# Kernel tuning notes

Measured on AMD Instinct MI355X. Metric: run time of the kernel, lower is better.

The kernel has to match this reference:

```python
import jax, jax.numpy as jnp
import numpy as np

P = 2048       # output dim (genes)
D = 64         # latent dim
H1, H2 = 512, 512  # n_neurons
E = 16         # num_experts
N = 2048       # batch
GATE_H = 64    # gate hidden width


def _glorot(key, shape):
    fan_in, fan_out = shape[-2], shape[-1]
    lim = jnp.sqrt(6.0 / (fan_in + fan_out)).astype(jnp.float32)
    return jax.random.uniform(key, shape, jnp.float32, -lim, lim)


def setup_inputs() -> dict:
    key = jax.random.key(0)
    ks = jax.random.split(key, 12)
    z = jax.random.normal(ks[0], (N, D), jnp.float32)
    # stacked per-expert MLP weights: d -> H1 -> H2 -> p
    W1 = _glorot(ks[1], (E, D, H1));  b1 = jnp.zeros((E, H1), jnp.float32)
    W2 = _glorot(ks[2], (E, H1, H2)); b2 = jnp.zeros((E, H2), jnp.float32)
    W3 = _glorot(ks[3], (E, H2, P));  b3 = jnp.zeros((E, P), jnp.float32)
    # gate network: d -> 64 -> E
    Wg1 = _glorot(ks[4], (D, GATE_H)); bg1 = jnp.zeros((GATE_H,), jnp.float32)
    Wg2 = _glorot(ks[5], (GATE_H, E)); bg2 = jnp.zeros((E,), jnp.float32)
    # expert assignment matrix A: [p, E], binary; ensure no all-zero row
    u = jax.random.uniform(ks[6], (P, E))
    A = jnp.where(u < 0.5, 1.0, 0.0).astype(jnp.float32)
    A = A.at[:, 0].set(1.0)
    return {"z": z, "W1": W1, "b1": b1, "W2": W2, "b2": b2,
            "W3": W3, "b3": b3, "Wg1": Wg1, "bg1": bg1,
            "Wg2": Wg2, "bg2": bg2, "A": A}


def reference(z, W1, b1, W2, b2, W3, b3, Wg1, bg1, Wg2, bg2, A):
    # experts, batched across E (replaces Python loop over nn.ModuleList)
    h = jax.nn.relu(jnp.einsum('nd,edh->neh', z, W1) + b1[None])      # [N,E,H1]
    h = jax.nn.relu(jnp.einsum('neh,ehk->nek', h, W2) + b2[None])     # [N,E,H2]
    expert_out = jnp.einsum('nek,ekp->nep', h, W3) + b3[None]         # [N,E,P]
    # gate network + softmax over experts
    g = jax.nn.relu(z @ Wg1 + bg1) @ Wg2 + bg2                        # [N,E]
    gate = jax.nn.softmax(g, axis=1)                                  # [N,E]
    # feature-wise gating: gate[n,e] * A[p,e], normalized over experts
    fw = gate[:, None, :] * A[None, :, :]                             # [N,P,E]
    fw = fw / (jnp.sum(fw, axis=2, keepdims=True) + 1e-8)
    # weighted combine: sum_e expert_out[n,e,p] * fw[n,p,e]
    x_rec = jnp.einsum('nep,npe->np', expert_out, fw)                 # [N,P]
    return (x_rec, fw)
```

## Files before the change

kernel.cpp:

```cpp
#include <hip/hip_runtime.h>
#include <hip/hip_bf16.h>

#define NN   2048
#define DD   64
#define HH1  512
#define HH2  512
#define PP   2048
#define EE   16

typedef unsigned short ushort_t;
typedef __attribute__((ext_vector_type(8))) short bf16x8;
typedef __attribute__((ext_vector_type(4))) float f32x4;

__device__ __forceinline__ float b2f(ushort_t u) {
  union { unsigned int i; float f; } v; v.i = ((unsigned int)u) << 16; return v.f;
}
__device__ __forceinline__ ushort_t f2b(float f) {
  union { float f; unsigned int i; } v; v.f = f;
  unsigned int x = v.i;
  unsigned int r = (x + 0x7fffu + ((x >> 16) & 1u)) >> 16;
  return (ushort_t)r;
}
__device__ __forceinline__ float ldf(const void* p, size_t i, int isb) {
  return isb ? b2f(((const ushort_t*)p)[i]) : ((const float*)p)[i];
}

__device__ __forceinline__ void async16(ushort_t* lds, const ushort_t* g) {
  __builtin_amdgcn_global_load_lds(
      (const __attribute__((address_space(1))) void*)g,
      (__attribute__((address_space(3))) void*)lds, 16, 0, 0);
}

__global__ void k_sniff(const unsigned int* __restrict__ zraw,
                        int* __restrict__ flag) {
  __shared__ int cnt[256];
  int t = threadIdx.x;
  int c = 0;
  for (int i = t; i < 1024; i += 256) {
    unsigned int u = zraw[i];
    unsigned int e = (u >> 7) & 0xFFu;
    c += (e >= 110u && e <= 135u) ? 1 : 0;
  }
  cnt[t] = c;
  __syncthreads();
  for (int s = 128; s > 0; s >>= 1) {
    if (t < s) cnt[t] += cnt[t + s];
    __syncthreads();
  }
  if (t == 0) *flag = (cnt[0] >= 512) ? 1 : 0;
}

__global__ void k_probe(int* __restrict__ mapflag) {
  __shared__ ushort_t Ap[16 * 32];
  __shared__ ushort_t Bp[16 * 32];
  int t = threadIdx.x;
  for (int i = t; i < 512; i += 64) {
    int r = i >> 5, k = i & 31;
    Ap[i] = f2b((float)((r + k) % 7));
    Bp[i] = f2b((float)((2 * r + k) % 5));
  }
  __syncthreads();
  int lr = t & 15, quad = t >> 4;
  bf16x8 a = *(const bf16x8*)&Ap[lr * 32 + quad * 8];
  bf16x8 b = *(const bf16x8*)&Bp[lr * 32 + quad * 8];
  f32x4 acc = {};
  acc = __builtin_amdgcn_mfma_f32_16x16x32_bf16(a, b, acc, 0, 0, 0);
  bool m0 = true, m1 = true;
  for (int r = 0; r < 4; ++r) {
    float r0 = 0.f, r1 = 0.f;
    for (int k = 0; k < 32; ++k) {
      r0 += (float)(((quad * 4 + r) + k) % 7) * (float)((2 * lr + k) % 5);
      r1 += (float)((lr + k) % 7) * (float)((2 * (quad * 4 + r) + k) % 5);
    }
    m0 &= fabsf(acc[r] - r0) < 0.5f;
    m1 &= fabsf(acc[r] - r1) < 0.5f;
  }
  unsigned long long b0 = __ballot(m0);
  unsigned long long b1 = __ballot(m1);
  if (t == 0) *mapflag = (b0 == ~0ULL) ? 0 : ((b1 == ~0ULL) ? 1 : 0);
}

__global__ void k_convert(const void* __restrict__ src,
                          ushort_t* __restrict__ dst, int n,
                          const int* __restrict__ flag) {
  int isb = *flag;
  int stride = gridDim.x * blockDim.x;
  for (int g = blockIdx.x * blockDim.x + threadIdx.x; g * 8 < n; g += stride) {
    int base = g * 8;
    ushort_t ov[8];
    if (isb) {
      *(uint4*)ov = *(const uint4*)((const ushort_t*)src + base);
    } else {
      const float* s = (const float*)src + base;
      float4 f0 = *(const float4*)s;
      float4 f1 = *(const float4*)(s + 4);
      ov[0] = f2b(f0.x); ov[1] = f2b(f0.y); ov[2] = f2b(f0.z); ov[3] = f2b(f0.w);
      ov[4] = f2b(f1.x); ov[5] = f2b(f1.y); ov[6] = f2b(f1.z); ov[7] = f2b(f1.w);
    }
    *(uint4*)(dst + base) = *(uint4*)ov;
  }
}

__global__ void k_transpose_cvt(const void* __restrict__ src_,
                                ushort_t* __restrict__ dst, int K, int H,
                                const int* __restrict__ flag) {
  __shared__ ushort_t tile[64][68];
  int isb = *flag;
  int e = blockIdx.z;
  size_t ebase = (size_t)e * K * H;
  dst += ebase;
  int h0 = blockIdx.x * 64, k0 = blockIdx.y * 64;
  int t = threadIdx.x;
#pragma unroll
  for (int it = 0; it < 2; ++it) {
    int c = it * 256 + t;
    int row = c >> 3, col = (c & 7) * 8;
    size_t idx = ebase + (size_t)(k0 + row) * H + h0 + col;
    ushort_t tmp[8];
    if (isb) {
      *(uint4*)tmp = *(const uint4*)((const ushort_t*)src_ + idx);
    } else {
      const float* s = (const float*)src_ + idx;
      float4 f0 = *(const float4*)s;
      float4 f1 = *(const float4*)(s + 4);
      tmp[0] = f2b(f0.x); tmp[1] = f2b(f0.y); tmp[2] = f2b(f0.z); tmp[3] = f2b(f0.w);
      tmp[4] = f2b(f1.x); tmp[5] = f2b(f1.y); tmp[6] = f2b(f1.z); tmp[7] = f2b(f1.w);
    }
#pragma unroll
    for (int j = 0; j < 8; ++j) tile[row][col + j] = tmp[j];
  }
  __syncthreads();
#pragma unroll
  for (int it = 0; it < 2; ++it) {
    int c = it * 256 + t;
    int row = c >> 3, col = (c & 7) * 8;
    ushort_t tmp[8];
#pragma unroll
    for (int j = 0; j < 8; ++j) tmp[j] = tile[col + j][row];
    *(uint4*)(dst + (size_t)(h0 + row) * K + k0 + col) = *(uint4*)tmp;
  }
}

__global__ void k_gate(const void* __restrict__ z,
                       const void* __restrict__ Wg1,
                       const void* __restrict__ bg1,
                       const void* __restrict__ Wg2,
                       const void* __restrict__ bg2,
                       const int* __restrict__ flag,
                       float* __restrict__ gate) {
  __shared__ float sW1[64][65];
  __shared__ float sW2[64][16];
  __shared__ float sb1[64];
  __shared__ float sb2[16];
  __shared__ float sz[4][64];
  __shared__ float shid[4][64];
  __shared__ float sg[4][16];
  int isb = *flag;
  int t = threadIdx.x;
  for (int i = t; i < 64 * 64; i += 256) sW1[i >> 6][i & 63] = ldf(Wg1, i, isb);
  for (int i = t; i < 64 * 16; i += 256) sW2[i >> 4][i & 15] = ldf(Wg2, i, isb);
  if (t < 64) sb1[t] = ldf(bg1, t, isb);
  if (t < 16) sb2[t] = ldf(bg2, t, isb);
  int w = t >> 6, l = t & 63;
  int n = blockIdx.x * 4 + w;
  sz[w][l] = ldf(z, (size_t)n * DD + l, isb);
  __syncthreads();
  float acc = sb1[l];
#pragma unroll
  for (int d = 0; d < 64; ++d) acc += sz[w][d] * sW1[d][l];
  shid[w][l] = fmaxf(acc, 0.f);
  __syncthreads();
  if (l < 16) {
    float g = sb2[l];
#pragma unroll
    for (int j = 0; j < 64; ++j) g += shid[w][j] * sW2[j][l];
    sg[w][l] = g;
  }
  __syncthreads();
  if (l < 16) {
    float m = -1e30f;
    for (int e2 = 0; e2 < 16; ++e2) m = fmaxf(m, sg[w][e2]);
    float s = 0.f;
    for (int e2 = 0; e2 < 16; ++e2) s += __expf(sg[w][e2] - m);
    gate[(size_t)n * EE + l] = __expf(sg[w][l] - m) / s;
  }
}

__global__ __launch_bounds__(256) void k_gemm_bt_relu(
    const ushort_t* __restrict__ Aact, const ushort_t* __restrict__ Bt,
    const ushort_t* __restrict__ bias, ushort_t* __restrict__ Cout,
    int M, int Nout, int K,
    long a_stride_e, long b_stride_e, long bias_stride_e, long c_stride_e,
    const int* __restrict__ mapflag) {
  __shared__ ushort_t As[128 * 32];
  __shared__ ushort_t Bs[128 * 32];
  int e = blockIdx.z;
  Aact += (size_t)e * a_stride_e;
  Bt   += (size_t)e * b_stride_e;
  bias += (size_t)e * bias_stride_e;
  Cout += (size_t)e * c_stride_e;
  int m0 = blockIdx.y * 128, n0 = blockIdx.x * 128;
  int t = threadIdx.x;
  int w = t >> 6, l = t & 63;
  int wm = (w >> 1) * 64, wn = (w & 1) * 64;
  int lr = l & 15, quad = l >> 4;
  int mf = *mapflag;

  f32x4 acc[4][4] = {};
  for (int k0 = 0; k0 < K; k0 += 32) {
#pragma unroll
    for (int it = 0; it < 2; ++it) {
      int c = it * 256 + t;
      int row = c >> 2, kk = (c & 3) * 8;
      async16(&As[row * 32 + kk], Aact + (size_t)(m0 + row) * K + k0 + kk);
    }
#pragma unroll
    for (int it = 0; it < 2; ++it) {
      int c = it * 256 + t;
      int row = c >> 2, kk = (c & 3) * 8;
      async16(&Bs[row * 32 + kk], Bt + (size_t)(n0 + row) * K + k0 + kk);
    }
    __syncthreads();
    bf16x8 af[4], bfr[4];
#pragma unroll
    for (int i = 0; i < 4; ++i)
      af[i] = *(const bf16x8*)&As[(wm + i * 16 + lr) * 32 + quad * 8];
#pragma unroll
    for (int j = 0; j < 4; ++j)
      bfr[j] = *(const bf16x8*)&Bs[(wn + j * 16 + lr) * 32 + quad * 8];
#pragma unroll
    for (int i = 0; i < 4; ++i)
#pragma unroll
      for (int j = 0; j < 4; ++j)
        acc[i][j] = __builtin_amdgcn_mfma_f32_16x16x32_bf16(af[i], bfr[j],
                                                            acc[i][j], 0, 0, 0);
    __syncthreads();
  }
  if (mf == 0) {
#pragma unroll
    for (int j = 0; j < 4; ++j) {
      int n = n0 + wn + j * 16 + lr;
      float bv = b2f(bias[n]);
#pragma unroll
      for (int i = 0; i < 4; ++i)
#pragma unroll
        for (int r = 0; r < 4; ++r) {
          int m = m0 + wm + i * 16 + quad * 4 + r;
          Cout[(size_t)m * Nout + n] = f2b(fmaxf(acc[i][j][r] + bv, 0.f));
        }
    }
  } else {
#pragma unroll
    for (int i = 0; i < 4; ++i) {
      int m = m0 + wm + i * 16 + lr;
#pragma unroll
      for (int j = 0; j < 4; ++j)
#pragma unroll
        for (int r = 0; r < 4; ++r) {
          int n = n0 + wn + j * 16 + quad * 4 + r;
          Cout[(size_t)m * Nout + n] = f2b(fmaxf(acc[i][j][r] + b2f(bias[n]), 0.f));
        }
    }
  }
}

__global__ __launch_bounds__(512) void k_l3_combine(
    const ushort_t* __restrict__ h2,
    const ushort_t* __restrict__ W3t,
    const ushort_t* __restrict__ b3,
    const ushort_t* __restrict__ Amat,
    const float* __restrict__ gate,
    float* __restrict__ xrec,
    const int* __restrict__ mapflag) {
  __shared__ ushort_t As[128 * 32];
  __shared__ ushort_t Bs[128 * 32];
  __shared__ float sGate[128][17];
  __shared__ float sA[128][17];
  __shared__ float sB3[16][132];
  int t = threadIdx.x;
  int n0 = blockIdx.y * 128, p0 = blockIdx.x * 128;
  for (int i = t; i < 128 * 16; i += 512) {
    int r = i >> 4, e2 = i & 15;
    sGate[r][e2] = gate[(size_t)(n0 + r) * EE + e2];
    sA[r][e2] = b2f(Amat[(size_t)(p0 + r) * EE + e2]);
  }
  for (int i = t; i < 16 * 128; i += 512) {
    int e2 = i >> 7, c = i & 127;
    sB3[e2][c] = b2f(b3[(size_t)e2 * PP + p0 + c]);
  }
  __syncthreads();
  int w = t >> 6, l = t & 63;
  int wm = (w >> 2) * 64, wn = (w & 3) * 32;
  int lr = l & 15, quad = l >> 4;
  int srow = t >> 2, skk = (t & 3) * 8;
  int mf = *mapflag;

  float weighted[4][2][4] = {};
  float denom[4][2][4] = {};
  for (int e = 0; e < EE; ++e) {
    f32x4 acc[4][2] = {};
    const ushort_t* h2e = h2 + (size_t)e * NN * HH2;
    const ushort_t* w3e = W3t + (size_t)e * PP * HH2;
    for (int k0 = 0; k0 < HH2; k0 += 32) {
      async16(&As[srow * 32 + skk], h2e + (size_t)(n0 + srow) * HH2 + k0 + skk);
      async16(&Bs[srow * 32 + skk], w3e + (size_t)(p0 + srow) * HH2 + k0 + skk);
      __syncthreads();
      bf16x8 af[4], bfr[2];
#pragma unroll
      for (int i = 0; i < 4; ++i)
        af[i] = *(const bf16x8*)&As[(wm + i * 16 + lr) * 32 + quad * 8];
#pragma unroll
      for (int j = 0; j < 2; ++j)
        bfr[j] = *(const bf16x8*)&Bs[(wn + j * 16 + lr) * 32 + quad * 8];
#pragma unroll
      for (int i = 0; i < 4; ++i)
#pragma unroll
        for (int j = 0; j < 2; ++j)
          acc[i][j] = __builtin_amdgcn_mfma_f32_16x16x32_bf16(
              af[i], bfr[j], acc[i][j], 0, 0, 0);
      __syncthreads();
    }
    if (mf == 0) {
#pragma unroll
      for (int i = 0; i < 4; ++i) {
        float g[4];
#pragma unroll
        for (int r = 0; r < 4; ++r) g[r] = sGate[wm + i * 16 + quad * 4 + r][e];
#pragma unroll
        for (int j = 0; j < 2; ++j) {
          int pl = wn + j * 16 + lr;
          float a = sA[pl][e];
          float bb = sB3[e][pl];
#pragma unroll
          for (int r = 0; r < 4; ++r) {
            float wgt = g[r] * a;
            weighted[i][j][r] += wgt * (acc[i][j][r] + bb);
            denom[i][j][r] += wgt;
          }
        }
      }
    } else {
#pragma unroll
      for (int i = 0; i < 4; ++i) {
        float gsc = sGate[wm + i * 16 + lr][e];
#pragma unroll
        for (int j = 0; j < 2; ++j)
#pragma unroll
          for (int r = 0; r < 4; ++r) {
            int pl = wn + j * 16 + quad * 4 + r;
            float wgt = gsc * sA[pl][e];
            weighted[i][j][r] += wgt * (acc[i][j][r] + sB3[e][pl]);
            denom[i][j][r] += wgt;
          }
      }
    }
  }
  if (mf == 0) {
#pragma unroll
    for (int j = 0; j < 2; ++j) {
      int p = p0 + wn + j * 16 + lr;
#pragma unroll
      for (int i = 0; i < 4; ++i)
#pragma unroll
        for (int r = 0; r < 4; ++r) {
          int n = n0 + wm + i * 16 + quad * 4 + r;
          xrec[(size_t)n * PP + p] = weighted[i][j][r] / (denom[i][j][r] + 1e-8f);
        }
    }
  } else {
#pragma unroll
    for (int i = 0; i < 4; ++i) {
      int n = n0 + wm + i * 16 + lr;
#pragma unroll
      for (int j = 0; j < 2; ++j)
#pragma unroll
        for (int r = 0; r < 4; ++r) {
          int p = p0 + wn + j * 16 + quad * 4 + r;
          xrec[(size_t)n * PP + p] = weighted[i][j][r] / (denom[i][j][r] + 1e-8f);
        }
    }
  }
}

__global__ void k_fw(const float* __restrict__ gate,
                     const ushort_t* __restrict__ Amat,
                     float* __restrict__ fw) {
  __shared__ float sg[16];
  int n = blockIdx.y;
  int p = blockIdx.x * 256 + threadIdx.x;
  if (threadIdx.x < 16) sg[threadIdx.x] = gate[(size_t)n * EE + threadIdx.x];
  __syncthreads();
  uint4 a0 = *(const uint4*)(Amat + (size_t)p * EE);
  uint4 a1 = *(const uint4*)(Amat + (size_t)p * EE + 8);
  ushort_t av[16];
  *(uint4*)av = a0;
  *(uint4*)(av + 8) = a1;
  float wv[16];
  float s = 0.f;
#pragma unroll
  for (int e = 0; e < 16; ++e) {
    wv[e] = sg[e] * b2f(av[e]);
    s += wv[e];
  }
  float inv = 1.f / (s + 1e-8f);
  float* dst = fw + ((size_t)n * PP + p) * EE;
#pragma unroll
  for (int e = 0; e < 16; ++e) wv[e] *= inv;
  *(float4*)(dst + 0)  = *(float4*)(wv + 0);
  *(float4*)(dst + 4)  = *(float4*)(wv + 4);
  *(float4*)(dst + 8)  = *(float4*)(wv + 8);
  *(float4*)(dst + 12) = *(float4*)(wv + 12);
}

extern "C" void kernel_launch(void* const* d_in, const int* in_sizes, int n_in,
                              void* d_out, int out_size, void* d_ws,
                              size_t ws_size, hipStream_t stream) {
  const void* z_r   = d_in[0];
  const void* W1_r  = d_in[1];
  const void* b1_r  = d_in[2];
  const void* W2_r  = d_in[3];
  const void* b2_r  = d_in[4];
  const void* W3_r  = d_in[5];
  const void* b3_r  = d_in[6];
  const void* Wg1_r = d_in[7];
  const void* bg1_r = d_in[8];
  const void* Wg2_r = d_in[9];
  const void* bg2_r = d_in[10];
  const void* A_r   = d_in[11];

  float* xrec = (float*)d_out;
  float* fw   = (float*)d_out + (size_t)NN * PP;

  char* ws = (char*)d_ws;
  int* flag    = (int*)ws;             ws += 128;
  int* mapflag = (int*)ws;             ws += 128;
  float* gate = (float*)ws;            ws += (size_t)NN * EE * 4;
  ushort_t* zC   = (ushort_t*)ws;      ws += (size_t)NN * DD * 2;
  ushort_t* b1C  = (ushort_t*)ws;      ws += (size_t)EE * HH1 * 2;
  ushort_t* b2C  = (ushort_t*)ws;      ws += (size_t)EE * HH2 * 2;
  ushort_t* b3C  = (ushort_t*)ws;      ws += (size_t)EE * PP * 2;
  ushort_t* AC   = (ushort_t*)ws;      ws += (size_t)PP * EE * 2;
  ushort_t* W1t = (ushort_t*)ws;       ws += (size_t)EE * HH1 * DD * 2;
  ushort_t* W2t = (ushort_t*)ws;       ws += (size_t)EE * HH2 * HH1 * 2;
  ushort_t* W3t = (ushort_t*)ws;       ws += (size_t)EE * PP * HH2 * 2;
  ushort_t* h1  = (ushort_t*)ws;       ws += (size_t)EE * NN * HH1 * 2;
  ushort_t* h2  = (ushort_t*)ws;       ws += (size_t)EE * NN * HH2 * 2;

  k_sniff<<<1, 256, 0, stream>>>((const unsigned int*)z_r, flag);
  k_probe<<<1, 64, 0, stream>>>(mapflag);

  auto cvt = [&](const void* src, ushort_t* dst, int n) {
    int blocks = (n / 8 + 255) / 256;
    if (blocks < 1) blocks = 1;
    k_convert<<<blocks, 256, 0, stream>>>(src, dst, n, flag);
  };
  cvt(z_r,  zC,  NN * DD);
  cvt(b1_r, b1C, EE * HH1);
  cvt(b2_r, b2C, EE * HH2);
  cvt(b3_r, b3C, EE * PP);
  cvt(A_r,  AC,  PP * EE);

  k_transpose_cvt<<<dim3(HH1 / 64, DD / 64, EE), 256, 0, stream>>>(
      W1_r, W1t, DD, HH1, flag);
  k_transpose_cvt<<<dim3(HH2 / 64, HH1 / 64, EE), 256, 0, stream>>>(
      W2_r, W2t, HH1, HH2, flag);
  k_transpose_cvt<<<dim3(PP / 64, HH2 / 64, EE), 256, 0, stream>>>(
      W3_r, W3t, HH2, PP, flag);

  k_gate<<<NN / 4, 256, 0, stream>>>(z_r, Wg1_r, bg1_r, Wg2_r, bg2_r, flag, gate);

  k_gemm_bt_relu<<<dim3(HH1 / 128, NN / 128, EE), 256, 0, stream>>>(
      zC, W1t, b1C, h1, NN, HH1, DD, 0, (long)HH1 * DD, HH1, (long)NN * HH1,
      mapflag);
  k_gemm_bt_relu<<<dim3(HH2 / 128, NN / 128, EE), 256, 0, stream>>>(
      h1, W2t, b2C, h2, NN, HH2, HH1, (long)NN * HH1, (long)HH2 * HH1, HH2,
      (long)NN * HH2, mapflag);

  k_l3_combine<<<dim3(PP / 128, NN / 128), 512, 0, stream>>>(
      h2, W3t, b3C, AC, gate, xrec, mapflag);

  k_fw<<<dim3(PP / 256, NN), 256, 0, stream>>>(gate, AC, fw);
}
```

Before: 642.6 us.

## Fold gate and A mask into operands, run layer 3 as one big-K split GEMM

Rewrites the layer-3 expert combine as a single GEMM with K = E*H2. The gate is scaled into the layer-2 output, which is written into a concatenated H2big buffer, and the A mask is multiplied into a concatenated W3 during transpose. The K dimension is split in two, and a final fused kernel sums the partials, adds the gated bias and normalizes while also writing fw. This removes the per-expert epilogue work and the lower-occupancy 512-thread combine kernel. In exchange it adds bf16 rounding of the gate-scaled activations, a fp32 partial buffer round trip and an extra reduction.

Result: faster. 600.3 us (-6.6%).

```diff
diff --git a/kernel.cpp b/kernel.cpp
--- a/kernel.cpp
+++ b/kernel.cpp
@@ -7,6 +7,8 @@
 #define HH2  512
 #define PP   2048
 #define EE   16
+#define KBIG (EE * HH2)
+#define SPLITS 2
 
 typedef unsigned short ushort_t;
 typedef __attribute__((ext_vector_type(8))) short bf16x8;
@@ -103,12 +105,14 @@
 
 __global__ void k_transpose_cvt(const void* __restrict__ src_,
                                 ushort_t* __restrict__ dst, int K, int H,
+                                int ld_dst, long e_dst_off,
+                                const void* __restrict__ Amask,
                                 const int* __restrict__ flag) {
   __shared__ ushort_t tile[64][68];
   int isb = *flag;
   int e = blockIdx.z;
   size_t ebase = (size_t)e * K * H;
-  dst += ebase;
+  dst += (size_t)e * e_dst_off;
   int h0 = blockIdx.x * 64, k0 = blockIdx.y * 64;
   int t = threadIdx.x;
 #pragma unroll
@@ -137,7 +141,12 @@
     ushort_t tmp[8];
 #pragma unroll
     for (int j = 0; j < 8; ++j) tmp[j] = tile[col + j][row];
-    *(uint4*)(dst + (size_t)(h0 + row) * K + k0 + col) = *(uint4*)tmp;
+    if (Amask) {
+      float a = ldf(Amask, (size_t)(h0 + row) * EE + e, isb);
+#pragma unroll
+      for (int j = 0; j < 8; ++j) tmp[j] = f2b(a * b2f(tmp[j]));
+    }
+    *(uint4*)(dst + (size_t)(h0 + row) * ld_dst + k0 + col) = *(uint4*)tmp;
   }
 }
 
@@ -189,8 +198,9 @@
 __global__ __launch_bounds__(256) void k_gemm_bt_relu(
     const ushort_t* __restrict__ Aact, const ushort_t* __restrict__ Bt,
     const ushort_t* __restrict__ bias, ushort_t* __restrict__ Cout,
-    int M, int Nout, int K,
+    int M, int K, int ldc,
     long a_stride_e, long b_stride_e, long bias_stride_e, long c_stride_e,
+    const float* __restrict__ gs,
     const int* __restrict__ mapflag) {
   __shared__ ushort_t As[128 * 32];
   __shared__ ushort_t Bs[128 * 32];
@@ -237,6 +247,13 @@
     __syncthreads();
   }
   if (mf == 0) {
+    float gv[4][4];
+#pragma unroll
+    for (int i = 0; i < 4; ++i)
+#pragma unroll
+      for (int r = 0; r < 4; ++r)
+        gv[i][r] = gs ? gs[(size_t)(m0 + wm + i * 16 + quad * 4 + r) * EE + e]
+                      : 1.f;
 #pragma unroll
     for (int j = 0; j < 4; ++j) {
       int n = n0 + wn + j * 16 + lr;
@@ -246,145 +263,107 @@
 #pragma unroll
         for (int r = 0; r < 4; ++r) {
           int m = m0 + wm + i * 16 + quad * 4 + r;
-          Cout[(size_t)m * Nout + n] = f2b(fmaxf(acc[i][j][r] + bv, 0.f));
+          Cout[(size_t)m * ldc + n] =
+              f2b(fmaxf(acc[i][j][r] + bv, 0.f) * gv[i][r]);
         }
     }
   } else {
 #pragma unroll
     for (int i = 0; i < 4; ++i) {
       int m = m0 + wm + i * 16 + lr;
+      float gvi = gs ? gs[(size_t)m * EE + e] : 1.f;
 #pragma unroll
       for (int j = 0; j < 4; ++j)
 #pragma unroll
         for (int r = 0; r < 4; ++r) {
           int n = n0 + wn + j * 16 + quad * 4 + r;
-          Cout[(size_t)m * Nout + n] = f2b(fmaxf(acc[i][j][r] + b2f(bias[n]), 0.f));
+          Cout[(size_t)m * ldc + n] =
+              f2b(fmaxf(acc[i][j][r] + b2f(bias[n]), 0.f) * gvi);
         }
     }
   }
 }
 
-__global__ __launch_bounds__(512) void k_l3_combine(
-    const ushort_t* __restrict__ h2,
-    const ushort_t* __restrict__ W3t,
-    const ushort_t* __restrict__ b3,
-    const ushort_t* __restrict__ Amat,
-    const float* __restrict__ gate,
-    float* __restrict__ xrec,
+__global__ __launch_bounds__(256) void k_bigk(
+    const ushort_t* __restrict__ Ab,
+    const ushort_t* __restrict__ Bb,
+    float* __restrict__ part,
     const int* __restrict__ mapflag) {
   __shared__ ushort_t As[128 * 32];
   __shared__ ushort_t Bs[128 * 32];
-  __shared__ float sGate[128][17];
-  __shared__ float sA[128][17];
-  __shared__ float sB3[16][132];
-  int t = threadIdx.x;
-  int n0 = blockIdx.y * 128, p0 = blockIdx.x * 128;
-  for (int i = t; i < 128 * 16; i += 512) {
-    int r = i >> 4, e2 = i & 15;
-    sGate[r][e2] = gate[(size_t)(n0 + r) * EE + e2];
-    sA[r][e2] = b2f(Amat[(size_t)(p0 + r) * EE + e2]);
-  }
-  for (int i = t; i < 16 * 128; i += 512) {
-    int e2 = i >> 7, c = i & 127;
-    sB3[e2][c] = b2f(b3[(size_t)e2 * PP + p0 + c]);
-  }
-  __syncthreads();
+  int s = blockIdx.z;
+  int m0 = blockIdx.y * 128, n0 = blockIdx.x * 128;
+  int t = threadIdx.x;
   int w = t >> 6, l = t & 63;
-  int wm = (w >> 2) * 64, wn = (w & 3) * 32;
+  int wm = (w >> 1) * 64, wn = (w & 1) * 64;
   int lr = l & 15, quad = l >> 4;
-  int srow = t >> 2, skk = (t & 3) * 8;
   int mf = *mapflag;
-
-  float weighted[4][2][4] = {};
-  float denom[4][2][4] = {};
-  for (int e = 0; e < EE; ++e) {
-    f32x4 acc[4][2] = {};
-    const ushort_t* h2e = h2 + (size_t)e * NN * HH2;
-    const ushort_t* w3e = W3t + (size_t)e * PP * HH2;
-    for (int k0 = 0; k0 < HH2; k0 += 32) {
-      async16(&As[srow * 32 + skk], h2e + (size_t)(n0 + srow) * HH2 + k0 + skk);
-      async16(&Bs[srow * 32 + skk], w3e + (size_t)(p0 + srow) * HH2 + k0 + skk);
-      __syncthreads();
-      bf16x8 af[4], bfr[2];
+  float* out = part + (size_t)s * NN * PP;
+  int kbeg = s * (KBIG / SPLITS), kend = kbeg + KBIG / SPLITS;
+
+  f32x4 acc[4][4] = {};
+  for (int k0 = kbeg; k0 < kend; k0 += 32) {
+#pragma unroll
+    for (int it = 0; it < 2; ++it) {
+      int c = it * 256 + t;
+      int row = c >> 2, kk = (c & 3) * 8;
+      async16(&As[row * 32 + kk], Ab + (size_t)(m0 + row) * KBIG + k0 + kk);
+    }
+#pragma unroll
+    for (int it = 0; it < 2; ++it) {
+      int c = it * 256 + t;
+      int row = c >> 2, kk = (c & 3) * 8;
+      async16(&Bs[row * 32 + kk], Bb + (size_t)(n0 + row) * KBIG + k0 + kk);
+    }
+    __syncthreads();
+    bf16x8 af[4], bfr[4];
+#pragma unroll
+    for (int i = 0; i < 4; ++i)
+      af[i] = *(const bf16x8*)&As[(wm + i * 16 + lr) * 32 + quad * 8];
+#pragma unroll
+    for (int j = 0; j < 4; ++j)
+      bfr[j] = *(const bf16x8*)&Bs[(wn + j * 16 + lr) * 32 + quad * 8];
+#pragma unroll
+    for (int i = 0; i < 4; ++i)
+#pragma unroll
+      for (int j = 0; j < 4; ++j)
+        acc[i][j] = __builtin_amdgcn_mfma_f32_16x16x32_bf16(af[i], bfr[j],
+                                                            acc[i][j], 0, 0, 0);
+    __syncthreads();
+  }
+  if (mf == 0) {
+#pragma unroll
+    for (int j = 0; j < 4; ++j) {
+      int n = n0 + wn + j * 16 + lr;
 #pragma unroll
       for (int i = 0; i < 4; ++i)
-        af[i] = *(const bf16x8*)&As[(wm + i * 16 + lr) * 32 + quad * 8];
-#pragma unroll
-      for (int j = 0; j < 2; ++j)
-        bfr[j] = *(const bf16x8*)&Bs[(wn + j * 16 + lr) * 32 + quad * 8];
-#pragma unroll
-      for (int i = 0; i < 4; ++i)
-#pragma unroll
-        for (int j = 0; j < 2; ++j)
-          acc[i][j] = __builtin_amdgcn_mfma_f32_16x16x32_bf16(
-              af[i], bfr[j], acc[i][j], 0, 0, 0);
-      __syncthreads();
-    }
-    if (mf == 0) {
-#pragma unroll
-      for (int i = 0; i < 4; ++i) {
-        float g[4];
-#pragma unroll
-        for (int r = 0; r < 4; ++r) g[r] = sGate[wm + i * 16 + quad * 4 + r][e];
-#pragma unroll
-        for (int j = 0; j < 2; ++j) {
-          int pl = wn + j * 16 + lr;
-          float a = sA[pl][e];
-          float bb = sB3[e][pl];
-#pragma unroll
-          for (int r = 0; r < 4; ++r) {
-            float wgt = g[r] * a;
-            weighted[i][j][r] += wgt * (acc[i][j][r] + bb);
-            denom[i][j][r] += wgt;
-          }
+#pragma unroll
+        for (int r = 0; r < 4; ++r) {
+          int m = m0 + wm + i * 16 + quad * 4 + r;
+          out[(size_t)m * PP + n] = acc[i][j][r];
         }
-      }
-    } else {
-#pragma unroll
-      for (int i = 0; i < 4; ++i) {
-        float gsc = sGate[wm + i * 16 + lr][e];
-#pragma unroll
-        for (int j = 0; j < 2; ++j)
-#pragma unroll
-          for (int r = 0; r < 4; ++r) {
-            int pl = wn + j * 16 + quad * 4 + r;
-            float wgt = gsc * sA[pl][e];
-            weighted[i][j][r] += wgt * (acc[i][j][r] + sB3[e][pl]);
-            denom[i][j][r] += wgt;
-          }
-      }
-    }
-  }
-  if (mf == 0) {
-#pragma unroll
-    for (int j = 0; j < 2; ++j) {
-      int p = p0 + wn + j * 16 + lr;
-#pragma unroll
-      for (int i = 0; i < 4; ++i)
+    }
+  } else {
+#pragma unroll
+    for (int i = 0; i < 4; ++i) {
+      int m = m0 + wm + i * 16 + lr;
+#pragma unroll
+      for (int j = 0; j < 4; ++j)
 #pragma unroll
         for (int r = 0; r < 4; ++r) {
-          int n = n0 + wm + i * 16 + quad * 4 + r;
-          xrec[(size_t)n * PP + p] = weighted[i][j][r] / (denom[i][j][r] + 1e-8f);
+          int n = n0 + wn + j * 16 + quad * 4 + r;
+          out[(size_t)m * PP + n] = acc[i][j][r];
         }
     }
-  } else {
-#pragma unroll
-    for (int i = 0; i < 4; ++i) {
-      int n = n0 + wm + i * 16 + lr;
-#pragma unroll
-      for (int j = 0; j < 2; ++j)
-#pragma unroll
-        for (int r = 0; r < 4; ++r) {
-          int p = p0 + wn + j * 16 + quad * 4 + r;
-          xrec[(size_t)n * PP + p] = weighted[i][j][r] / (denom[i][j][r] + 1e-8f);
-        }
-    }
-  }
-}
-
-__global__ void k_fw(const float* __restrict__ gate,
-                     const ushort_t* __restrict__ Amat,
-                     float* __restrict__ fw) {
+  }
+}
+
+__global__ void k_fw_final(const float* __restrict__ gate,
+                           const ushort_t* __restrict__ Amat,
+                           const ushort_t* __restrict__ b3,
+                           const float* __restrict__ part,
+                           float* __restrict__ xrec,
+                           float* __restrict__ fw) {
   __shared__ float sg[16];
   int n = blockIdx.y;
   int p = blockIdx.x * 256 + threadIdx.x;
@@ -396,14 +375,18 @@
   *(uint4*)av = a0;
   *(uint4*)(av + 8) = a1;
   float wv[16];
-  float s = 0.f;
+  float s = 0.f, bias = 0.f;
 #pragma unroll
   for (int e = 0; e < 16; ++e) {
     wv[e] = sg[e] * b2f(av[e]);
     s += wv[e];
+    bias += wv[e] * b2f(b3[(size_t)e * PP + p]);
   }
   float inv = 1.f / (s + 1e-8f);
-  float* dst = fw + ((size_t)n * PP + p) * EE;
+  size_t np = (size_t)n * PP + p;
+  float num = part[np] + part[(size_t)NN * PP + np] + bias;
+  xrec[np] = num * inv;
+  float* dst = fw + np * EE;
 #pragma unroll
   for (int e = 0; e < 16; ++e) wv[e] *= inv;
   *(float4*)(dst + 0)  = *(float4*)(wv + 0);
@@ -442,9 +425,10 @@
   ushort_t* AC   = (ushort_t*)ws;      ws += (size_t)PP * EE * 2;
   ushort_t* W1t = (ushort_t*)ws;       ws += (size_t)EE * HH1 * DD * 2;
   ushort_t* W2t = (ushort_t*)ws;       ws += (size_t)EE * HH2 * HH1 * 2;
-  ushort_t* W3t = (ushort_t*)ws;       ws += (size_t)EE * PP * HH2 * 2;
+  ushort_t* W3big = (ushort_t*)ws;     ws += (size_t)PP * KBIG * 2;
+  ushort_t* H2big = (ushort_t*)ws;     ws += (size_t)NN * KBIG * 2;
   ushort_t* h1  = (ushort_t*)ws;       ws += (size_t)EE * NN * HH1 * 2;
-  ushort_t* h2  = (ushort_t*)ws;       ws += (size_t)EE * NN * HH2 * 2;
+  float* partial = (float*)h1;
 
   k_sniff<<<1, 256, 0, stream>>>((const unsigned int*)z_r, flag);
   k_probe<<<1, 64, 0, stream>>>(mapflag);
@@ -461,23 +445,24 @@
   cvt(A_r,  AC,  PP * EE);
 
   k_transpose_cvt<<<dim3(HH1 / 64, DD / 64, EE), 256, 0, stream>>>(
-      W1_r, W1t, DD, HH1, flag);
+      W1_r, W1t, DD, HH1, DD, (long)HH1 * DD, nullptr, flag);
   k_transpose_cvt<<<dim3(HH2 / 64, HH1 / 64, EE), 256, 0, stream>>>(
-      W2_r, W2t, HH1, HH2, flag);
+      W2_r, W2t, HH1, HH2, HH1, (long)HH2 * HH1, nullptr, flag);
   k_transpose_cvt<<<dim3(PP / 64, HH2 / 64, EE), 256, 0, stream>>>(
-      W3_r, W3t, HH2, PP, flag);
+      W3_r, W3big, HH2, PP, KBIG, (long)HH2, A_r, flag);
 
   k_gate<<<NN / 4, 256, 0, stream>>>(z_r, Wg1_r, bg1_r, Wg2_r, bg2_r, flag, gate);
 
   k_gemm_bt_relu<<<dim3(HH1 / 128, NN / 128, EE), 256, 0, stream>>>(
-      zC, W1t, b1C, h1, NN, HH1, DD, 0, (long)HH1 * DD, HH1, (long)NN * HH1,
-      mapflag);
+      zC, W1t, b1C, h1, NN, DD, HH1,
+      0, (long)HH1 * DD, HH1, (long)NN * HH1, nullptr, mapflag);
   k_gemm_bt_relu<<<dim3(HH2 / 128, NN / 128, EE), 256, 0, stream>>>(
-      h1, W2t, b2C, h2, NN, HH2, HH1, (long)NN * HH1, (long)HH2 * HH1, HH2,
-      (long)NN * HH2, mapflag);
-
-  k_l3_combine<<<dim3(PP / 128, NN / 128), 512, 0, stream>>>(
-      h2, W3t, b3C, AC, gate, xrec, mapflag);
-
-  k_fw<<<dim3(PP / 256, NN), 256, 0, stream>>>(gate, AC, fw);
-}
+      h1, W2t, b2C, H2big, NN, HH1, KBIG,
+      (long)NN * HH1, (long)HH2 * HH1, HH2, (long)HH2, gate, mapflag);
+
+  k_bigk<<<dim3(PP / 128, NN / 128, SPLITS), 256, 0, stream>>>(
+      H2big, W3big, partial, mapflag);
+
+  k_fw_final<<<dim3(PP / 256, NN), 256, 0, stream>>>(
+      gate, AC, b3C, partial, xrec, fw);
+}
```
